# Kernel tuning notes

Measured on AMD Instinct MI355X. Metric: run time of the kernel, lower is better.

## Reference

```python
import jax, jax.numpy as jnp
import numpy as np


def setup_inputs() -> dict:
    key = jax.random.key(0)
    kq, kk, kv = jax.random.split(key, 3)
    shape = (4, 8, 64, 8192)  # (b, n_heads, d, s)
    q = jax.random.normal(kq, shape, dtype=jnp.float32)
    k = jax.random.normal(kk, shape, dtype=jnp.float32)
    v = jax.random.normal(kv, shape, dtype=jnp.float32)
    return {"q": q, "k": k, "v": v}


def reference(q, k, v):
    # q, k, v: (b, n, d, s)
    q = jax.nn.softmax(q, axis=-2)        # softmax over feature dim d
    k = jax.nn.softmax(k, axis=-1)        # softmax over sequence dim s
    scale = q.shape[-2] ** (-0.5)
    q = q * scale
    # context: (b, n, d_k, d_v) = sum_s k[..., i, s] * v[..., j, s]
    context = jnp.einsum('bnis,bnjs->bnij', k, v)
    # out: (b, n, d_v, s)
    out = jnp.einsum('bnij,bnis->bnjs', context, q)
    return out
```

## Files before the change

kernel.cpp:

```cpp
#include <hip/hip_runtime.h>
#include <stdint.h>


typedef __attribute__((ext_vector_type(8))) short bf16x8;
typedef __attribute__((ext_vector_type(4))) float floatx4;

constexpr int D = 64, S = 8192, HEADS = 32;
constexpr int NC = 16;
constexpr int CHUNK = S / NC;
constexpr int NT = CHUNK / 64;

__device__ __forceinline__ short bf16_rn(float x) {
    unsigned u = __builtin_bit_cast(unsigned, x);
    return (short)((u + 0x8000u) >> 16);
}
__device__ __forceinline__ float bf16_f(short h) {
    unsigned u = ((unsigned)(unsigned short)h) << 16;
    return __builtin_bit_cast(float, u);
}
__device__ __forceinline__ void split8(const float* x, bf16x8& hi, bf16x8& lo) {
#pragma unroll
    for (int e = 0; e < 8; ++e) {
        short h = bf16_rn(x[e]);
        hi[e] = h;
        lo[e] = bf16_rn(x[e] - bf16_f(h));
    }
}

__device__ __forceinline__ void gl16(const void* g, void* l) {
    __builtin_amdgcn_global_load_lds(
        (const __attribute__((address_space(1))) unsigned int*)g,
        (__attribute__((address_space(3))) unsigned int*)l, 16, 0, 0);
}

__global__ __launch_bounds__(512, 4) void ctx_kernel(
    const float* __restrict__ K, const float* __restrict__ V,
    float* __restrict__ Cpart,
    float* __restrict__ Rpart)
{
    __shared__ char smem[2 * 2 * 16384];
    const int h = blockIdx.x, c = blockIdx.y;
    const int wave = threadIdx.x >> 6, lane = threadIdx.x & 63;
    const int m = lane & 15, quad = lane >> 4;

    const float* Kb = K + (size_t)h * D * S;
    const float* Vb = V + (size_t)h * D * S;
    const int c0 = c * CHUNK;

    const int ii = wave << 2;
    const int smat = ii >> 4;
    const int r0base = (ii & 15) << 2;
    const float* gmat = smat ? Vb : Kb;

    auto stage = [&](int buf, int t) {
        const int colf = c0 + (t << 6);
#pragma unroll
        for (int g = 0; g < 4; ++g) {
            const int r0 = r0base + (g << 2);
            const int r = r0 + (lane >> 4);
            const int su = (lane & 15) ^ (r & 7);
            const float* src = gmat + (size_t)r * S + colf + (su << 2);
            char* dst = smem + (buf << 15) + (smat << 14) + (r0 << 8);
            gl16(src, dst);
        }
    };

    const int mt = wave >> 1, nt0 = (wave & 1) << 1;
    const int rA = mt * 16 + m;
    floatx4 acc[2];
    acc[0] = (floatx4){0.f, 0.f, 0.f, 0.f};
    acc[1] = (floatx4){0.f, 0.f, 0.f, 0.f};
    float rs = 0.f;

    stage(0, 0);
    for (int t = 0; t < NT; ++t) {
        if (t + 1 < NT) {
            stage((t + 1) & 1, t + 1);
            asm volatile("s_waitcnt vmcnt(4)" ::: "memory");
        } else {
            asm volatile("s_waitcnt vmcnt(0)" ::: "memory");
        }
        asm volatile("s_barrier" ::: "memory");

        const char* kb = smem + ((t & 1) << 15);
        const char* vb = kb + 16384;
#pragma unroll
        for (int ks = 0; ks < 2; ++ks) {
            const int u0 = (ks << 3) + (quad << 1);
            float ar[8];
            const char* kr = kb + (rA << 8);
            *(float4*)&ar[0] = *(const float4*)(kr + ((u0 ^ (rA & 7)) << 4));
            *(float4*)&ar[4] = *(const float4*)(kr + (((u0 + 1) ^ (rA & 7)) << 4));
            float ex[8];
#pragma unroll
            for (int e = 0; e < 8; ++e) {
                ex[e] = __expf(ar[e]);
                rs += ex[e];
            }
            bf16x8 ah, al;
            split8(ex, ah, al);
#pragma unroll
            for (int j = 0; j < 2; ++j) {
                const int rB = (nt0 + j) * 16 + m;
                float br[8];
                const char* vr = vb + (rB << 8);
                *(float4*)&br[0] = *(const float4*)(vr + ((u0 ^ (rB & 7)) << 4));
                *(float4*)&br[4] = *(const float4*)(vr + (((u0 + 1) ^ (rB & 7)) << 4));
                bf16x8 bh, bl;
                split8(br, bh, bl);
                acc[j] = __builtin_amdgcn_mfma_f32_16x16x32_bf16(ah, bh, acc[j], 0, 0, 0);
                acc[j] = __builtin_amdgcn_mfma_f32_16x16x32_bf16(ah, bl, acc[j], 0, 0, 0);
                acc[j] = __builtin_amdgcn_mfma_f32_16x16x32_bf16(al, bh, acc[j], 0, 0, 0);
            }
        }
        asm volatile("s_barrier" ::: "memory");
    }

    rs += __shfl_xor(rs, 16, 64);
    rs += __shfl_xor(rs, 32, 64);

    const size_t pbase = (((size_t)h * NC + c) << 12);
#pragma unroll
    for (int j = 0; j < 2; ++j)
#pragma unroll
        for (int r = 0; r < 4; ++r)
            Cpart[pbase + ((size_t)(((mt * 4 + nt0 + j) * 4 + r)) << 6) + lane] =
                acc[j][r];
    if ((wave & 1) == 0 && lane < 16)
        Rpart[(((size_t)h * NC + c) << 6) + mt * 16 + lane] = rs;
}

__global__ __launch_bounds__(256) void reduce_kernel(
    const float* __restrict__ Cpart, const float* __restrict__ Rpart,
    float* __restrict__ CnT)
{
    __shared__ float invr[D];
    const int h = blockIdx.x, p = blockIdx.y, t = threadIdx.x;

    if (t < D) {
        float s = 0.f;
#pragma unroll
        for (int c = 0; c < NC; ++c)
            s += Rpart[(((size_t)h * NC + c) << 6) + t];
        invr[t] = 0.125f / s;
    }
    __syncthreads();

#pragma unroll
    for (int k = 0; k < 2; ++k) {
        const int idx = (p << 9) + (k << 8) + t;
        float s = 0.f;
#pragma unroll
        for (int c = 0; c < NC; ++c)
            s += Cpart[(((size_t)h * NC + c) << 12) + idx];
        const int tile = idx >> 8, reg = (idx >> 6) & 3, lane = idx & 63;
        const int mtl = tile >> 2, ntl = tile & 3;
        const int i = mtl * 16 + ((lane >> 4) << 2) + reg;
        const int j = ntl * 16 + (lane & 15);
        CnT[((size_t)h << 12) + j * 64 + i] = s * invr[i];
    }
}

__global__ __launch_bounds__(256) void out_kernel(
    const float* __restrict__ Q, const float* __restrict__ CnT,
    float* __restrict__ Out)
{
    const int h = blockIdx.x;
    const int wave = threadIdx.x >> 6, lane = threadIdx.x & 63;
    const int m = lane & 15, quad = lane >> 4;
    const int sbase = (blockIdx.y * 4 + wave) * 128;

    bf16x8 Ah[4][2], Al[4][2];
    const float* Cb = CnT + (size_t)h * 4096;
#pragma unroll
    for (int jt = 0; jt < 4; ++jt)
#pragma unroll
        for (int kk = 0; kk < 2; ++kk) {
            float a[8];
            const float* p = Cb + (jt * 16 + m) * 64 + kk * 32 + quad * 8;
            *(float4*)&a[0] = *(const float4*)p;
            *(float4*)&a[4] = *(const float4*)(p + 4);
            split8(a, Ah[jt][kk], Al[jt][kk]);
        }

    const float* Qb = Q + (size_t)h * D * S;
    float* Ob = Out + (size_t)h * D * S;

    for (int it = 0; it < 8; ++it) {
        const int scol = sbase + it * 16 + m;
        float e[16];
        float cs = 0.f;
#pragma unroll
        for (int kk = 0; kk < 2; ++kk)
#pragma unroll
            for (int j2 = 0; j2 < 8; ++j2) {
                const float qv = Qb[(size_t)(kk * 32 + quad * 8 + j2) * S + scol];
                const float ev = __expf(qv);
                e[kk * 8 + j2] = ev;
                cs += ev;
            }
        cs += __shfl_xor(cs, 16, 64);
        cs += __shfl_xor(cs, 32, 64);
        const float inv = 1.0f / cs;

        bf16x8 Bh[2], Bl[2];
        split8(&e[0], Bh[0], Bl[0]);
        split8(&e[8], Bh[1], Bl[1]);

#pragma unroll
        for (int jt = 0; jt < 4; ++jt) {
            floatx4 a = (floatx4){0.f, 0.f, 0.f, 0.f};
#pragma unroll
            for (int kk = 0; kk < 2; ++kk) {
                a = __builtin_amdgcn_mfma_f32_16x16x32_bf16(Ah[jt][kk], Bh[kk], a, 0, 0, 0);
                a = __builtin_amdgcn_mfma_f32_16x16x32_bf16(Ah[jt][kk], Bl[kk], a, 0, 0, 0);
                a = __builtin_amdgcn_mfma_f32_16x16x32_bf16(Al[jt][kk], Bh[kk], a, 0, 0, 0);
            }
#pragma unroll
            for (int r = 0; r < 4; ++r)
                Ob[(size_t)(jt * 16 + quad * 4 + r) * S + scol] = a[r] * inv;
        }
    }
}

extern "C" void kernel_launch(void* const* d_in, const int* in_sizes, int n_in,
                              void* d_out, int out_size, void* d_ws, size_t ws_size,
                              hipStream_t stream) {
    const float* q = (const float*)d_in[0];
    const float* k = (const float*)d_in[1];
    const float* v = (const float*)d_in[2];
    float* out = (float*)d_out;

    float* Cpart = (float*)d_ws;
    float* Rpart = Cpart + (size_t)HEADS * NC * 4096;
    float* CnT   = Rpart + (size_t)HEADS * NC * 64;

    ctx_kernel<<<dim3(HEADS, NC), 512, 0, stream>>>(k, v, Cpart, Rpart);
    reduce_kernel<<<dim3(HEADS, 8), 256, 0, stream>>>(Cpart, Rpart, CnT);
    out_kernel<<<dim3(HEADS, 16), 256, 0, stream>>>(q, CnT, out);
}
```

Baseline: 253.3 us.

## Replace LDS-staged context kernel with direct register double-buffered global loads

The context kernel no longer stages K and V tiles through LDS with global_load_lds and barriers. Each of four waves now loads its K and V rows straight from global memory into registers, double-buffered across 32-column steps, and computes a 2x2 block of MFMA tiles. This also exposes exp(K) reuse across two V tiles. The chunk count doubles to 32 and blocks shrink to 256 threads, which gives more blocks. The partial buffer and the reduce work double, and the per-lane strided 32-byte global loads may coalesce worse than the LDS path did.

```diff
diff --git a/kernel.cpp b/kernel.cpp
--- a/kernel.cpp
+++ b/kernel.cpp
@@ -6,9 +6,9 @@
 typedef __attribute__((ext_vector_type(4))) float floatx4;
 
 constexpr int D = 64, S = 8192, HEADS = 32;
-constexpr int NC = 16;
+constexpr int NC = 32;
 constexpr int CHUNK = S / NC;
-constexpr int NT = CHUNK / 64;
+constexpr int NK = CHUNK / 32;
 
 __device__ __forceinline__ short bf16_rn(float x) {
     unsigned u = __builtin_bit_cast(unsigned, x);
@@ -27,107 +27,105 @@
     }
 }
 
-__device__ __forceinline__ void gl16(const void* g, void* l) {
-    __builtin_amdgcn_global_load_lds(
-        (const __attribute__((address_space(1))) unsigned int*)g,
-        (__attribute__((address_space(3))) unsigned int*)l, 16, 0, 0);
-}
-
-__global__ __launch_bounds__(512, 4) void ctx_kernel(
+__global__ __launch_bounds__(256, 3) void ctx_kernel(
     const float* __restrict__ K, const float* __restrict__ V,
     float* __restrict__ Cpart,
     float* __restrict__ Rpart)
 {
-    __shared__ char smem[2 * 2 * 16384];
     const int h = blockIdx.x, c = blockIdx.y;
     const int wave = threadIdx.x >> 6, lane = threadIdx.x & 63;
     const int m = lane & 15, quad = lane >> 4;
-
-    const float* Kb = K + (size_t)h * D * S;
-    const float* Vb = V + (size_t)h * D * S;
-    const int c0 = c * CHUNK;
-
-    const int ii = wave << 2;
-    const int smat = ii >> 4;
-    const int r0base = (ii & 15) << 2;
-    const float* gmat = smat ? Vb : Kb;
-
-    auto stage = [&](int buf, int t) {
-        const int colf = c0 + (t << 6);
-#pragma unroll
-        for (int g = 0; g < 4; ++g) {
-            const int r0 = r0base + (g << 2);
-            const int r = r0 + (lane >> 4);
-            const int su = (lane & 15) ^ (r & 7);
-            const float* src = gmat + (size_t)r * S + colf + (su << 2);
-            char* dst = smem + (buf << 15) + (smat << 14) + (r0 << 8);
-            gl16(src, dst);
+    const int wr = wave >> 1, wc = wave & 1;
+
+    const float* Kb = K + (size_t)h * D * S + (c * CHUNK + quad * 8);
+    const float* Vb = V + (size_t)h * D * S + (c * CHUNK + quad * 8);
+
+    const float* pa[2];
+    const float* pb[2];
+#pragma unroll
+    for (int x = 0; x < 2; ++x) {
+        pa[x] = Kb + (size_t)((wr * 2 + x) * 16 + m) * S;
+        pb[x] = Vb + (size_t)((wc * 2 + x) * 16 + m) * S;
+    }
+
+    floatx4 acc[2][2];
+#pragma unroll
+    for (int a = 0; a < 2; ++a)
+#pragma unroll
+        for (int b = 0; b < 2; ++b) acc[a][b] = (floatx4){0.f, 0.f, 0.f, 0.f};
+    float rs[2] = {0.f, 0.f};
+
+    float ka0[2][8], va0[2][8], ka1[2][8], va1[2][8];
+
+    auto loadstep = [&](float (*ka)[8], float (*va)[8], int kk) {
+        const int off = kk * 32;
+#pragma unroll
+        for (int x = 0; x < 2; ++x) {
+            *(float4*)&ka[x][0] = *(const float4*)(pa[x] + off);
+            *(float4*)&ka[x][4] = *(const float4*)(pa[x] + off + 4);
+            *(float4*)&va[x][0] = *(const float4*)(pb[x] + off);
+            *(float4*)&va[x][4] = *(const float4*)(pb[x] + off + 4);
         }
     };
 
-    const int mt = wave >> 1, nt0 = (wave & 1) << 1;
-    const int rA = mt * 16 + m;
-    floatx4 acc[2];
-    acc[0] = (floatx4){0.f, 0.f, 0.f, 0.f};
-    acc[1] = (floatx4){0.f, 0.f, 0.f, 0.f};
-    float rs = 0.f;
-
-    stage(0, 0);
-    for (int t = 0; t < NT; ++t) {
-        if (t + 1 < NT) {
-            stage((t + 1) & 1, t + 1);
-            asm volatile("s_waitcnt vmcnt(4)" ::: "memory");
-        } else {
-            asm volatile("s_waitcnt vmcnt(0)" ::: "memory");
-        }
-        asm volatile("s_barrier" ::: "memory");
-
-        const char* kb = smem + ((t & 1) << 15);
-        const char* vb = kb + 16384;
-#pragma unroll
-        for (int ks = 0; ks < 2; ++ks) {
-            const int u0 = (ks << 3) + (quad << 1);
-            float ar[8];
-            const char* kr = kb + (rA << 8);
-            *(float4*)&ar[0] = *(const float4*)(kr + ((u0 ^ (rA & 7)) << 4));
-            *(float4*)&ar[4] = *(const float4*)(kr + (((u0 + 1) ^ (rA & 7)) << 4));
+    auto compute = [&](float (*ka)[8], float (*va)[8]) {
+        bf16x8 ah[2], al[2], bh[2], bl[2];
+#pragma unroll
+        for (int x = 0; x < 2; ++x) {
             float ex[8];
 #pragma unroll
             for (int e = 0; e < 8; ++e) {
-                ex[e] = __expf(ar[e]);
-                rs += ex[e];
-            }
-            bf16x8 ah, al;
-            split8(ex, ah, al);
-#pragma unroll
-            for (int j = 0; j < 2; ++j) {
-                const int rB = (nt0 + j) * 16 + m;
-                float br[8];
-                const char* vr = vb + (rB << 8);
-                *(float4*)&br[0] = *(const float4*)(vr + ((u0 ^ (rB & 7)) << 4));
-                *(float4*)&br[4] = *(const float4*)(vr + (((u0 + 1) ^ (rB & 7)) << 4));
-                bf16x8 bh, bl;
-                split8(br, bh, bl);
-                acc[j] = __builtin_amdgcn_mfma_f32_16x16x32_bf16(ah, bh, acc[j], 0, 0, 0);
-                acc[j] = __builtin_amdgcn_mfma_f32_16x16x32_bf16(ah, bl, acc[j], 0, 0, 0);
-                acc[j] = __builtin_amdgcn_mfma_f32_16x16x32_bf16(al, bh, acc[j], 0, 0, 0);
-            }
-        }
-        asm volatile("s_barrier" ::: "memory");
-    }
-
-    rs += __shfl_xor(rs, 16, 64);
-    rs += __shfl_xor(rs, 32, 64);
-
-    const size_t pbase = (((size_t)h * NC + c) << 12);
-#pragma unroll
-    for (int j = 0; j < 2; ++j)
-#pragma unroll
-        for (int r = 0; r < 4; ++r)
-            Cpart[pbase + ((size_t)(((mt * 4 + nt0 + j) * 4 + r)) << 6) + lane] =
-                acc[j][r];
-    if ((wave & 1) == 0 && lane < 16)
-        Rpart[(((size_t)h * NC + c) << 6) + mt * 16 + lane] = rs;
+                ex[e] = __expf(ka[x][e]);
+                rs[x] += ex[e];
+            }
+            split8(ex, ah[x], al[x]);
+            split8(va[x], bh[x], bl[x]);
+        }
+#pragma unroll
+        for (int a = 0; a < 2; ++a)
+#pragma unroll
+            for (int b = 0; b < 2; ++b) {
+                acc[a][b] = __builtin_amdgcn_mfma_f32_16x16x32_bf16(
+                    ah[a], bh[b], acc[a][b], 0, 0, 0);
+                acc[a][b] = __builtin_amdgcn_mfma_f32_16x16x32_bf16(
+                    ah[a], bl[b], acc[a][b], 0, 0, 0);
+                acc[a][b] = __builtin_amdgcn_mfma_f32_16x16x32_bf16(
+                    al[a], bh[b], acc[a][b], 0, 0, 0);
+            }
+    };
+
+    loadstep(ka0, va0, 0);
+#pragma unroll
+    for (int kk = 0; kk < NK; kk += 2) {
+        if (kk + 1 < NK) loadstep(ka1, va1, kk + 1);
+        compute(ka0, va0);
+        if (kk + 2 < NK) loadstep(ka0, va0, kk + 2);
+        compute(ka1, va1);
+    }
+
+#pragma unroll
+    for (int x = 0; x < 2; ++x) {
+        float v0 = rs[x];
+        v0 += __shfl_xor(v0, 16, 64);
+        v0 += __shfl_xor(v0, 32, 64);
+        rs[x] = v0;
+    }
+
+    const size_t pbase = ((size_t)(h * NC + c)) << 12;
+#pragma unroll
+    for (int a = 0; a < 2; ++a)
+#pragma unroll
+        for (int b = 0; b < 2; ++b) {
+            const int tile = (wr * 2 + a) * 4 + (wc * 2 + b);
+#pragma unroll
+            for (int r = 0; r < 4; ++r)
+                Cpart[pbase + ((size_t)(tile * 4 + r) << 6) + lane] = acc[a][b][r];
+        }
+    if (wc == 0 && lane < 16) {
+#pragma unroll
+        for (int x = 0; x < 2; ++x)
+            Rpart[(((size_t)(h * NC + c)) << 6) + (wr * 2 + x) * 16 + lane] = rs[x];
+    }
 }
 
 __global__ __launch_bounds__(256) void reduce_kernel(
@@ -141,7 +139,7 @@
         float s = 0.f;
 #pragma unroll
         for (int c = 0; c < NC; ++c)
-            s += Rpart[(((size_t)h * NC + c) << 6) + t];
+            s += Rpart[(((size_t)(h * NC + c)) << 6) + t];
         invr[t] = 0.125f / s;
     }
     __syncthreads();
@@ -152,7 +150,7 @@
         float s = 0.f;
 #pragma unroll
         for (int c = 0; c < NC; ++c)
-            s += Cpart[(((size_t)h * NC + c) << 12) + idx];
+            s += Cpart[(((size_t)(h * NC + c)) << 12) + idx];
         const int tile = idx >> 8, reg = (idx >> 6) & 3, lane = idx & 63;
         const int mtl = tile >> 2, ntl = tile & 3;
         const int i = mtl * 16 + ((lane >> 4) << 2) + reg;
@@ -235,7 +233,7 @@
     float* Rpart = Cpart + (size_t)HEADS * NC * 4096;
     float* CnT   = Rpart + (size_t)HEADS * NC * 64;
 
-    ctx_kernel<<<dim3(HEADS, NC), 512, 0, stream>>>(k, v, Cpart, Rpart);
+    ctx_kernel<<<dim3(HEADS, NC), 256, 0, stream>>>(k, v, Cpart, Rpart);
     reduce_kernel<<<dim3(HEADS, 8), 256, 0, stream>>>(Cpart, Rpart, CnT);
     out_kernel<<<dim3(HEADS, 16), 256, 0, stream>>>(q, CnT, out);
 }
```

Measured after the change: 271.4 us. +7.1%, slower.
